# Kernel tuning notes

Measured on AMD Instinct MI355X. Metric: run time of the kernel, lower is better.

The kernel has to match this reference:

```python
import jax, jax.numpy as jnp
import numpy as np

B, T, C, D = 8, 4096, 1024, 128  # batch, seq_len, n_embd, attn_dim


def setup_inputs() -> dict:
    key = jax.random.key(0)
    kx, kq, kk, kv = jax.random.split(key, 4)
    scale = 0.02
    return {
        "x": jax.random.normal(kx, (B, T, C), dtype=jnp.float32),
        "Wq": jax.random.normal(kq, (C, D), dtype=jnp.float32) * scale,
        "Wk": jax.random.normal(kk, (C, D), dtype=jnp.float32) * scale,
        "Wv": jax.random.normal(kv, (C, D), dtype=jnp.float32) * scale,
    }


def reference(x, Wq, Wk, Wv):
    # single-head causal self-attention (dropout in eval mode -> identity)
    q = jnp.einsum("btc,cd->btd", x, Wq)
    k = jnp.einsum("btc,cd->btd", x, Wk)
    v = jnp.einsum("btc,cd->btd", x, Wv)
    dk = q.shape[-1]
    scores = jnp.einsum("btd,bsd->bts", q, k) / jnp.sqrt(jnp.float32(dk))  # [B,T,T]
    tq = q.shape[1]
    causal = jnp.tril(jnp.ones((tq, tq), dtype=bool))
    scores = jnp.where(causal[None, :, :], scores, jnp.float32(-jnp.inf))
    weights = jax.nn.softmax(scores, axis=-1)
    return jnp.einsum("bts,bsd->btd", weights, v)
```

## Files before the change

### kernel.cpp

```cpp
#include <hip/hip_runtime.h>
#include <hip/hip_bf16.h>
#include <stdint.h>


typedef __attribute__((ext_vector_type(8))) short short8;
typedef __attribute__((ext_vector_type(4))) float f32x4;
typedef __attribute__((ext_vector_type(4))) unsigned short u16x4;

#define NB 8
#define NT 4096
#define NC 1024
#define ND 128

__device__ __forceinline__ unsigned short f2bf(float f) {
    union { float f; uint32_t u; } v; v.f = f;
    uint32_t u = v.u;
    return (unsigned short)((u + 0x7FFFu + ((u >> 16) & 1u)) >> 16);
}

__global__ void prep_w(const float* __restrict__ Wq, const float* __restrict__ Wk,
                       const float* __restrict__ Wv, unsigned short* __restrict__ Wbt) {
    int idx = blockIdx.x * 256 + threadIdx.x;
    int w = idx >> 17;
    int rem = idx & 131071;
    int n = rem >> 10;
    int k = rem & 1023;
    const float* W = (w == 0) ? Wq : (w == 1) ? Wk : Wv;
    Wbt[idx] = f2bf(W[k * ND + n]);
}

__global__ __launch_bounds__(256, 3)
void qkv_gemm(const float* __restrict__ x, const unsigned short* __restrict__ Wbt,
              unsigned short* __restrict__ Qo, unsigned short* __restrict__ Ko,
              unsigned short* __restrict__ Vto) {
    __shared__ __align__(16) float Al[128 * 64];
    __shared__ __align__(16) unsigned short Bl[128 * 64];
    const int mt = blockIdx.x, nt = blockIdx.y;
    const int tid = threadIdx.x;
    const int lane = tid & 63;
    const int w = tid >> 6;
    const int wr = w >> 1, wc = w & 1;
    const int l15 = lane & 15, lg = lane >> 4;
    const int m0 = mt * 128;
    const unsigned short* Wn = Wbt + (size_t)nt * (ND * NC);

    f32x4 acc[4][4];
#pragma unroll
    for (int i = 0; i < 4; ++i)
#pragma unroll
        for (int j = 0; j < 4; ++j) acc[i][j] = (f32x4)0.0f;

    for (int ks = 0; ks < 16; ++ks) {
        const int k0 = ks * 64;
#pragma unroll
        for (int r = 0; r < 8; ++r) {
            int o = r * 4096 + tid * 16;
            int row = o >> 8;
            int colb = (o & 255) ^ ((row & 7) << 4);
            const float* src = x + (size_t)(m0 + row) * NC + k0 + (colb >> 2);
            __builtin_amdgcn_global_load_lds(
                (const __attribute__((address_space(1))) void*)src,
                (__attribute__((address_space(3))) void*)((char*)Al + o), 16, 0, 0);
        }
#pragma unroll
        for (int r = 0; r < 4; ++r) {
            int o = r * 4096 + tid * 16;
            int row = o >> 7;
            int colb = (o & 127) ^ ((row & 7) << 4);
            const unsigned short* src = Wn + (size_t)row * NC + k0 + (colb >> 1);
            __builtin_amdgcn_global_load_lds(
                (const __attribute__((address_space(1))) void*)src,
                (__attribute__((address_space(3))) void*)((char*)Bl + o), 16, 0, 0);
        }
        __syncthreads();

#pragma unroll
        for (int kc = 0; kc < 2; ++kc) {
            short8 a[4], b[4];
#pragma unroll
            for (int mi = 0; mi < 4; ++mi) {
                const int row = wr * 64 + mi * 16 + l15;
                const int cb = (row & 7) << 4;
                const int base = row * 256;
                f32x4 lo = *reinterpret_cast<const f32x4*>(
                    (const char*)Al + base + ((kc * 128 + lg * 32) ^ cb));
                f32x4 hi = *reinterpret_cast<const f32x4*>(
                    (const char*)Al + base + ((kc * 128 + lg * 32 + 16) ^ cb));
                short8 av;
#pragma unroll
                for (int e = 0; e < 4; ++e) {
                    av[e] = (short)f2bf(lo[e]);
                    av[4 + e] = (short)f2bf(hi[e]);
                }
                a[mi] = av;
            }
#pragma unroll
            for (int ni = 0; ni < 4; ++ni) {
                const int row = wc * 64 + ni * 16 + l15;
                const int cb = (row & 7) << 4;
                b[ni] = *reinterpret_cast<const short8*>(
                    (const char*)Bl + row * 128 + ((kc * 64 + lg * 16) ^ cb));
            }
#pragma unroll
            for (int mi = 0; mi < 4; ++mi)
#pragma unroll
                for (int ni = 0; ni < 4; ++ni)
                    acc[mi][ni] = __builtin_amdgcn_mfma_f32_16x16x32_bf16(
                        a[mi], b[ni], acc[mi][ni], 0, 0, 0);
        }
        __syncthreads();
    }
#pragma unroll
    for (int mi = 0; mi < 4; ++mi)
#pragma unroll
        for (int ni = 0; ni < 4; ++ni)
#pragma unroll
            for (int r = 0; r < 4; ++r) {
                int row = m0 + wr * 64 + mi * 16 + lg * 4 + r;
                int col = wc * 64 + ni * 16 + l15;
                float v = acc[mi][ni][r];
                if (nt == 0) v *= 0.08838834764831845f;
                unsigned short bv = f2bf(v);
                if (nt == 0) Qo[(size_t)row * ND + col] = bv;
                else if (nt == 1) Ko[(size_t)row * ND + col] = bv;
                else {
                    int bb2 = row >> 12, t = row & 4095;
                    Vto[((size_t)(bb2 * ND + col)) * NT + t] = bv;
                }
            }
}

__global__ __launch_bounds__(512, 2)
void attn_fwd(const unsigned short* __restrict__ Q, const unsigned short* __restrict__ K,
              const unsigned short* __restrict__ Vt, float* __restrict__ out) {
    __shared__ __align__(16) char smem[149504];

    const int bid = blockIdx.x;
    const int p = bid >> 3, b = bid & 7;
    const int tid = threadIdx.x;
    const int w = tid >> 6, lane = tid & 63;
    const int l15 = lane & 15, lg = lane >> 4;
    const int g = w >> 2, wq = w & 3;

    const float L2E = 1.4426950408889634f;

    unsigned short* Kg = (unsigned short*)(smem + g * 32768);
    unsigned short* Vg = (unsigned short*)(smem + 65536 + g * 32768);
    unsigned short* pw = (unsigned short*)(smem + 131072 + w * 2304);
    float* mOp = (float*)(smem) + wq * 2048;
    float* mml = (float*)(smem + 32768) + wq * 32;

    const unsigned short* Kbase = &K[(size_t)b * NT * ND];
    const unsigned short* Vbase = &Vt[(size_t)b * ND * NT];

    auto stage = [&](int buf, int s0) {
#pragma unroll
        for (int r = 0; r < 4; ++r) {
            int off = r * 4096 + wq * 1024 + lane * 16;
            int row = off >> 8;
            int gcol = (off & 255) ^ ((row & 7) << 4);
            const unsigned short* src = Kbase + (size_t)(s0 + row) * ND + (gcol >> 1);
            __builtin_amdgcn_global_load_lds(
                (const __attribute__((address_space(1))) void*)src,
                (__attribute__((address_space(3))) void*)(Kg + ((buf * 16384 + r * 4096 + wq * 1024) >> 1)),
                16, 0, 0);
        }
#pragma unroll
        for (int r = 0; r < 4; ++r) {
            int off = r * 4096 + wq * 1024 + lane * 16;
            int row = off >> 7;
            int gcol = (off & 127) ^ ((row & 7) << 4);
            const unsigned short* src = Vbase + (size_t)row * NT + s0 + (gcol >> 1);
            __builtin_amdgcn_global_load_lds(
                (const __attribute__((address_space(1))) void*)src,
                (__attribute__((address_space(3))) void*)(Vg + ((buf * 16384 + r * 4096 + wq * 1024) >> 1)),
                16, 0, 0);
        }
    };

    for (int half = 0; half < 2; ++half) {
        const int qt = half ? (63 - p) : p;
        const int qb0 = qt * 64;
        const int qw0 = qb0 + wq * 16;
        const int niter = (qt + 2) >> 1;

        short8 qf[4];
        const size_t qbase = ((size_t)b * NT + qw0 + l15) * ND;
#pragma unroll
        for (int c = 0; c < 4; ++c)
            qf[c] = *reinterpret_cast<const short8*>(&Q[qbase + c * 32 + lg * 8]);

        f32x4 o[8];
#pragma unroll
        for (int jn = 0; jn < 8; ++jn) o[jn] = (f32x4)0.0f;
        float mrow = -1e30f, lsum = 0.0f;

        if (g <= qt) stage(0, g * 64);
        __syncthreads();
        int cur = 0;

        for (int i = 0; i < niter; ++i) {
            const int t = 2 * i + g;
            const int s0 = t * 64;
            if (t + 2 <= qt) stage(cur ^ 1, (t + 2) * 64);

            if (t <= qt) {
                const unsigned short* KlC = Kg + cur * 8192;
                f32x4 s[4];
#pragma unroll
                for (int j = 0; j < 4; ++j) s[j] = (f32x4)0.0f;
                __builtin_amdgcn_s_setprio(1);
#pragma unroll
                for (int j = 0; j < 4; ++j) {
                    const int row = j * 16 + l15;
                    const int cb = (row & 7) << 4;
#pragma unroll
                    for (int c = 0; c < 4; ++c) {
                        short8 kf = *reinterpret_cast<const short8*>(
                            &KlC[row * 128 + (((c * 64 + lg * 16) ^ cb) >> 1)]);
                        s[j] = __builtin_amdgcn_mfma_f32_16x16x32_bf16(kf, qf[c], s[j], 0, 0, 0);
                    }
                }
                __builtin_amdgcn_s_setprio(0);

                const unsigned short* VlC = Vg + cur * 8192;
                short8 vf0[8];
#pragma unroll
                for (int jn = 0; jn < 4; ++jn) {
                    const int row = jn * 16 + l15;
                    const int cb = (row & 7) << 4;
#pragma unroll
                    for (int kc = 0; kc < 2; ++kc)
                        vf0[jn * 2 + kc] = *reinterpret_cast<const short8*>(
                            &VlC[row * 64 + (((kc * 64 + lg * 16) ^ cb) >> 1)]);
                }

                const bool diag = (s0 + 64 > qw0);
                float pmax = -1e30f;
                if (diag) {
#pragma unroll
                    for (int j = 0; j < 4; ++j)
#pragma unroll
                        for (int r = 0; r < 4; ++r) {
                            float sv = s[j][r];
                            if (s0 + j * 16 + lg * 4 + r > qw0 + l15) sv = -1e30f;
                            s[j][r] = sv;
                            pmax = fmaxf(pmax, sv);
                        }
                } else {
#pragma unroll
                    for (int j = 0; j < 4; ++j)
#pragma unroll
                        for (int r = 0; r < 4; ++r)
                            pmax = fmaxf(pmax, s[j][r]);
                }
                pmax = fmaxf(pmax, __shfl_xor(pmax, 16, 64));
                pmax = fmaxf(pmax, __shfl_xor(pmax, 32, 64));
                const bool need = (pmax > mrow + 8.0f);
                float mn = need ? pmax : mrow;
                float alpha = need ? exp2f((mrow - mn) * L2E) : 1.0f;
                mrow = mn;
                float psum = 0.0f;
#pragma unroll
                for (int j = 0; j < 4; ++j)
#pragma unroll
                    for (int r = 0; r < 4; ++r) {
                        float pv = exp2f((s[j][r] - mn) * L2E);
                        s[j][r] = pv;
                        psum += pv;
                    }
                psum += __shfl_xor(psum, 16, 64);
                psum += __shfl_xor(psum, 32, 64);
                lsum = lsum * alpha + psum;

#pragma unroll
                for (int j = 0; j < 4; ++j) {
                    uint2 val;
                    asm("v_cvt_pk_bf16_f32 %0, %1, %2"
                        : "=v"(val.x) : "v"(s[j][0]), "v"(s[j][1]));
                    asm("v_cvt_pk_bf16_f32 %0, %1, %2"
                        : "=v"(val.y) : "v"(s[j][2]), "v"(s[j][3]));
                    *reinterpret_cast<uint2*>(&pw[l15 * 72 + j * 16 + lg * 4]) = val;
                }
                asm volatile("s_waitcnt lgkmcnt(0)" ::: "memory");
                short8 pa[2];
#pragma unroll
                for (int kc = 0; kc < 2; ++kc)
                    pa[kc] = *reinterpret_cast<const short8*>(&pw[l15 * 72 + kc * 32 + lg * 8]);
                asm volatile("s_waitcnt lgkmcnt(0)" ::: "memory");

                if (__any((int)need)) {
                    float aT[4];
#pragma unroll
                    for (int r = 0; r < 4; ++r) aT[r] = __shfl(alpha, lg * 4 + r, 64);
#pragma unroll
                    for (int jn = 0; jn < 8; ++jn)
#pragma unroll
                        for (int r = 0; r < 4; ++r) o[jn][r] *= aT[r];
                }

                __builtin_amdgcn_s_setprio(1);
#pragma unroll
                for (int jn = 0; jn < 4; ++jn)
#pragma unroll
                    for (int kc = 0; kc < 2; ++kc)
                        o[jn] = __builtin_amdgcn_mfma_f32_16x16x32_bf16(
                            pa[kc], vf0[jn * 2 + kc], o[jn], 0, 0, 0);
#pragma unroll
                for (int jn = 4; jn < 8; ++jn) {
                    const int row = jn * 16 + l15;
                    const int cb = (row & 7) << 4;
#pragma unroll
                    for (int kc = 0; kc < 2; ++kc) {
                        short8 vf = *reinterpret_cast<const short8*>(
                            &VlC[row * 64 + (((kc * 64 + lg * 16) ^ cb) >> 1)]);
                        o[jn] = __builtin_amdgcn_mfma_f32_16x16x32_bf16(pa[kc], vf, o[jn], 0, 0, 0);
                    }
                }
                __builtin_amdgcn_s_setprio(0);
            }

            __syncthreads();
            cur ^= 1;
        }

        if (g == 1) {
#pragma unroll
            for (int jn = 0; jn < 8; ++jn)
#pragma unroll
                for (int r = 0; r < 4; ++r)
                    mOp[(lg * 4 + r) * 128 + jn * 16 + l15] = o[jn][r];
            if (lg == 0) {
                mml[l15] = mrow;
                mml[16 + l15] = lsum;
            }
        }
        __syncthreads();
        if (g == 0) {
            float e0[4], e1[4], rL[4];
#pragma unroll
            for (int r = 0; r < 4; ++r) {
                int rr = lg * 4 + r;
                float m0T = __shfl(mrow, rr, 64);
                float l0T = __shfl(lsum, rr, 64);
                float m1 = mml[rr], l1 = mml[16 + rr];
                float M = fmaxf(m0T, m1);
                e0[r] = exp2f((m0T - M) * L2E);
                e1[r] = exp2f((m1 - M) * L2E);
                rL[r] = 1.0f / (l0T * e0[r] + l1 * e1[r]);
            }
#pragma unroll
            for (int jn = 0; jn < 8; ++jn)
#pragma unroll
                for (int r = 0; r < 4; ++r) {
                    int rr = lg * 4 + r, cc = jn * 16 + l15;
                    float v = o[jn][r] * e0[r] + mOp[rr * 128 + cc] * e1[r];
                    out[((size_t)b * NT + qw0 + rr) * ND + cc] = v * rL[r];
                }
        }
        __syncthreads();
    }
}

extern "C" void kernel_launch(void* const* d_in, const int* in_sizes, int n_in,
                              void* d_out, int out_size, void* d_ws, size_t ws_size,
                              hipStream_t stream) {
    const float* x  = (const float*)d_in[0];
    const float* Wq = (const float*)d_in[1];
    const float* Wk = (const float*)d_in[2];
    const float* Wv = (const float*)d_in[3];
    float* out = (float*)d_out;

    unsigned short* ws  = (unsigned short*)d_ws;
    unsigned short* Wbt = ws;
    unsigned short* Qb  = Wbt + 3 * ND * NC;
    unsigned short* Kb  = Qb + (size_t)NB * NT * ND;
    unsigned short* Vtb = Kb + (size_t)NB * NT * ND;

    prep_w<<<1536, 256, 0, stream>>>(Wq, Wk, Wv, Wbt);
    qkv_gemm<<<dim3(256, 3), 256, 0, stream>>>(x, Wbt, Qb, Kb, Vtb);
    attn_fwd<<<256, 512, 0, stream>>>(Qb, Kb, Vtb, out);
}
```

Measured before the change: 130.3 us.

## Software-pipeline softmax/PV of previous tile behind QK^T of current tile

Restructures the attention inner loop so each iteration first runs softmax and the PV MFMAs for the previously computed score tile, then computes QK^T for the current tile and preloads all V fragments into registers. The aim is to overlap the MFMA score computation with the exp/reduction work, hiding latency within each wave. It raises register pressure (16 V fragments plus carried scores), which risks lower occupancy or spills.

```diff
diff --git a/kernel.cpp b/kernel.cpp
--- a/kernel.cpp
+++ b/kernel.cpp
@@ -195,6 +195,114 @@
         for (int jn = 0; jn < 8; ++jn) o[jn] = (f32x4)0.0f;
         float mrow = -1e30f, lsum = 0.0f;
 
+        f32x4 sp[4];
+        short8 vfp[16];
+        int s0p = -1;
+
+        auto QKT = [&](const unsigned short* KlC) {
+#pragma unroll
+            for (int j = 0; j < 4; ++j) sp[j] = (f32x4)0.0f;
+            __builtin_amdgcn_s_setprio(1);
+#pragma unroll
+            for (int j = 0; j < 4; ++j) {
+                const int row = j * 16 + l15;
+                const int cb = (row & 7) << 4;
+#pragma unroll
+                for (int c = 0; c < 4; ++c) {
+                    short8 kf = *reinterpret_cast<const short8*>(
+                        &KlC[row * 128 + (((c * 64 + lg * 16) ^ cb) >> 1)]);
+                    sp[j] = __builtin_amdgcn_mfma_f32_16x16x32_bf16(kf, qf[c], sp[j], 0, 0, 0);
+                }
+            }
+            __builtin_amdgcn_s_setprio(0);
+        };
+        auto readVF = [&](const unsigned short* VlC) {
+#pragma unroll
+            for (int jn = 0; jn < 8; ++jn) {
+                const int row = jn * 16 + l15;
+                const int cb = (row & 7) << 4;
+#pragma unroll
+                for (int kc = 0; kc < 2; ++kc)
+                    vfp[jn * 2 + kc] = *reinterpret_cast<const short8*>(
+                        &VlC[row * 64 + (((kc * 64 + lg * 16) ^ cb) >> 1)]);
+            }
+        };
+        auto SMPV = [&]() {
+            const int s0c = s0p;
+            const bool diag = (s0c + 64 > qw0);
+            float pmax = -1e30f;
+            if (diag) {
+#pragma unroll
+                for (int j = 0; j < 4; ++j)
+#pragma unroll
+                    for (int r = 0; r < 4; ++r) {
+                        float sv = sp[j][r];
+                        if (s0c + j * 16 + lg * 4 + r > qw0 + l15) sv = -1e30f;
+                        sp[j][r] = sv;
+                        pmax = fmaxf(pmax, sv);
+                    }
+            } else {
+#pragma unroll
+                for (int j = 0; j < 4; ++j)
+#pragma unroll
+                    for (int r = 0; r < 4; ++r)
+                        pmax = fmaxf(pmax, sp[j][r]);
+            }
+            pmax = fmaxf(pmax, __shfl_xor(pmax, 16, 64));
+            pmax = fmaxf(pmax, __shfl_xor(pmax, 32, 64));
+            const bool need = (pmax > mrow + 8.0f);
+            float mn = need ? pmax : mrow;
+            float alpha = need ? exp2f((mrow - mn) * L2E) : 1.0f;
+            mrow = mn;
+            float psum = 0.0f;
+#pragma unroll
+            for (int j = 0; j < 4; ++j)
+#pragma unroll
+                for (int r = 0; r < 4; ++r) {
+                    float pv = exp2f((sp[j][r] - mn) * L2E);
+                    sp[j][r] = pv;
+                    psum += pv;
+                }
+            psum += __shfl_xor(psum, 16, 64);
+            psum += __shfl_xor(psum, 32, 64);
+            lsum = lsum * alpha + psum;
+
+#pragma unroll
+            for (int j = 0; j < 4; ++j) {
+                uint2 val;
+                asm("v_cvt_pk_bf16_f32 %0, %1, %2"
+                    : "=v"(val.x) : "v"(sp[j][0]), "v"(sp[j][1]));
+                asm("v_cvt_pk_bf16_f32 %0, %1, %2"
+                    : "=v"(val.y) : "v"(sp[j][2]), "v"(sp[j][3]));
+                *reinterpret_cast<uint2*>(&pw[l15 * 72 + j * 16 + lg * 4]) = val;
+            }
+            asm volatile("s_waitcnt lgkmcnt(0)" ::: "memory");
+            short8 pa[2];
+#pragma unroll
+            for (int kc = 0; kc < 2; ++kc)
+                pa[kc] = *reinterpret_cast<const short8*>(&pw[l15 * 72 + kc * 32 + lg * 8]);
+            asm volatile("s_waitcnt lgkmcnt(0)" ::: "memory");
+
+            if (__any((int)need)) {
+                float aT[4];
+#pragma unroll
+                for (int r = 0; r < 4; ++r) aT[r] = __shfl(alpha, lg * 4 + r, 64);
+#pragma unroll
+                for (int jn = 0; jn < 8; ++jn)
+#pragma unroll
+                    for (int r = 0; r < 4; ++r) o[jn][r] *= aT[r];
+            }
+
+            __builtin_amdgcn_s_setprio(1);
+#pragma unroll
+            for (int jn = 0; jn < 8; ++jn)
+#pragma unroll
+                for (int kc = 0; kc < 2; ++kc)
+                    o[jn] = __builtin_amdgcn_mfma_f32_16x16x32_bf16(
+                        pa[kc], vfp[jn * 2 + kc], o[jn], 0, 0, 0);
+            __builtin_amdgcn_s_setprio(0);
+        };
+
         if (g <= qt) stage(0, g * 64);
         __syncthreads();
         int cur = 0;
@@ -204,125 +312,20 @@
             const int s0 = t * 64;
             if (t + 2 <= qt) stage(cur ^ 1, (t + 2) * 64);
 
+            if (s0p >= 0) SMPV();
+
             if (t <= qt) {
-                const unsigned short* KlC = Kg + cur * 8192;
-                f32x4 s[4];
-#pragma unroll
-                for (int j = 0; j < 4; ++j) s[j] = (f32x4)0.0f;
-                __builtin_amdgcn_s_setprio(1);
-#pragma unroll
-                for (int j = 0; j < 4; ++j) {
-                    const int row = j * 16 + l15;
-                    const int cb = (row & 7) << 4;
-#pragma unroll
-                    for (int c = 0; c < 4; ++c) {
-                        short8 kf = *reinterpret_cast<const short8*>(
-                            &KlC[row * 128 + (((c * 64 + lg * 16) ^ cb) >> 1)]);
-                        s[j] = __builtin_amdgcn_mfma_f32_16x16x32_bf16(kf, qf[c], s[j], 0, 0, 0);
-                    }
-                }
-                __builtin_amdgcn_s_setprio(0);
-
-                const unsigned short* VlC = Vg + cur * 8192;
-                short8 vf0[8];
-#pragma unroll
-                for (int jn = 0; jn < 4; ++jn) {
-                    const int row = jn * 16 + l15;
-                    const int cb = (row & 7) << 4;
-#pragma unroll
-                    for (int kc = 0; kc < 2; ++kc)
-                        vf0[jn * 2 + kc] = *reinterpret_cast<const short8*>(
-                            &VlC[row * 64 + (((kc * 64 + lg * 16) ^ cb) >> 1)]);
-                }
-
-                const bool diag = (s0 + 64 > qw0);
-                float pmax = -1e30f;
-                if (diag) {
-#pragma unroll
-                    for (int j = 0; j < 4; ++j)
-#pragma unroll
-                        for (int r = 0; r < 4; ++r) {
-                            float sv = s[j][r];
-                            if (s0 + j * 16 + lg * 4 + r > qw0 + l15) sv = -1e30f;
-                            s[j][r] = sv;
-                            pmax = fmaxf(pmax, sv);
-                        }
-                } else {
-#pragma unroll
-                    for (int j = 0; j < 4; ++j)
-#pragma unroll
-                        for (int r = 0; r < 4; ++r)
-                            pmax = fmaxf(pmax, s[j][r]);
-                }
-                pmax = fmaxf(pmax, __shfl_xor(pmax, 16, 64));
-                pmax = fmaxf(pmax, __shfl_xor(pmax, 32, 64));
-                const bool need = (pmax > mrow + 8.0f);
-                float mn = need ? pmax : mrow;
-                float alpha = need ? exp2f((mrow - mn) * L2E) : 1.0f;
-                mrow = mn;
-                float psum = 0.0f;
-#pragma unroll
-                for (int j = 0; j < 4; ++j)
-#pragma unroll
-                    for (int r = 0; r < 4; ++r) {
-                        float pv = exp2f((s[j][r] - mn) * L2E);
-                        s[j][r] = pv;
-                        psum += pv;
-                    }
-                psum += __shfl_xor(psum, 16, 64);
-                psum += __shfl_xor(psum, 32, 64);
-                lsum = lsum * alpha + psum;
-
-#pragma unroll
-                for (int j = 0; j < 4; ++j) {
-                    uint2 val;
-                    asm("v_cvt_pk_bf16_f32 %0, %1, %2"
-                        : "=v"(val.x) : "v"(s[j][0]), "v"(s[j][1]));
-                    asm("v_cvt_pk_bf16_f32 %0, %1, %2"
-                        : "=v"(val.y) : "v"(s[j][2]), "v"(s[j][3]));
-                    *reinterpret_cast<uint2*>(&pw[l15 * 72 + j * 16 + lg * 4]) = val;
-                }
-                asm volatile("s_waitcnt lgkmcnt(0)" ::: "memory");
-                short8 pa[2];
-#pragma unroll
-                for (int kc = 0; kc < 2; ++kc)
-                    pa[kc] = *reinterpret_cast<const short8*>(&pw[l15 * 72 + kc * 32 + lg * 8]);
-                asm volatile("s_waitcnt lgkmcnt(0)" ::: "memory");
-
-                if (__any((int)need)) {
-                    float aT[4];
-#pragma unroll
-                    for (int r = 0; r < 4; ++r) aT[r] = __shfl(alpha, lg * 4 + r, 64);
-#pragma unroll
-                    for (int jn = 0; jn < 8; ++jn)
-#pragma unroll
-                        for (int r = 0; r < 4; ++r) o[jn][r] *= aT[r];
-                }
-
-                __builtin_amdgcn_s_setprio(1);
-#pragma unroll
-                for (int jn = 0; jn < 4; ++jn)
-#pragma unroll
-                    for (int kc = 0; kc < 2; ++kc)
-                        o[jn] = __builtin_amdgcn_mfma_f32_16x16x32_bf16(
-                            pa[kc], vf0[jn * 2 + kc], o[jn], 0, 0, 0);
-#pragma unroll
-                for (int jn = 4; jn < 8; ++jn) {
-                    const int row = jn * 16 + l15;
-                    const int cb = (row & 7) << 4;
-#pragma unroll
-                    for (int kc = 0; kc < 2; ++kc) {
-                        short8 vf = *reinterpret_cast<const short8*>(
-                            &VlC[row * 64 + (((kc * 64 + lg * 16) ^ cb) >> 1)]);
-                        o[jn] = __builtin_amdgcn_mfma_f32_16x16x32_bf16(pa[kc], vf, o[jn], 0, 0, 0);
-                    }
-                }
-                __builtin_amdgcn_s_setprio(0);
+                QKT(Kg + cur * 8192);
+                readVF(Vg + cur * 8192);
+                s0p = s0;
+            } else {
+                s0p = -1;
             }
 
             __syncthreads();
             cur ^= 1;
         }
+        if (s0p >= 0) SMPV();
 
         if (g == 1) {
 #pragma unroll
```

Result: slower. 136.8 us (+5.0%).

## Fuse Q/K/V projections per block so each x tile is loaded once

Applied to the files above, without the earlier changes.

The QKV GEMM now computes all three projections in one block with a 64-row M tile and a 384-wide N tile, instead of launching a separate grid slice per projection. The goal is to read the fp32 x activations (the dominant traffic) and convert them to bf16 only once instead of three times. The cost is more weight traffic per block, a larger LDS footprint (48KB of weights plus 16KB of x), more accumulator registers, and lower occupancy (launch bounds drop from 3 to 2).

```diff
diff --git a/kernel.cpp b/kernel.cpp
--- a/kernel.cpp
+++ b/kernel.cpp
@@ -29,31 +29,32 @@
     Wbt[idx] = f2bf(W[k * ND + n]);
 }
 
-__global__ __launch_bounds__(256, 3)
+__global__ __launch_bounds__(256, 2)
 void qkv_gemm(const float* __restrict__ x, const unsigned short* __restrict__ Wbt,
               unsigned short* __restrict__ Qo, unsigned short* __restrict__ Ko,
               unsigned short* __restrict__ Vto) {
-    __shared__ __align__(16) float Al[128 * 64];
-    __shared__ __align__(16) unsigned short Bl[128 * 64];
-    const int mt = blockIdx.x, nt = blockIdx.y;
+    __shared__ __align__(16) float Al[64 * 64];
+    __shared__ __align__(16) unsigned short Bl[3 * 128 * 64];
+    const int mt = blockIdx.x;
     const int tid = threadIdx.x;
     const int lane = tid & 63;
     const int w = tid >> 6;
     const int wr = w >> 1, wc = w & 1;
     const int l15 = lane & 15, lg = lane >> 4;
-    const int m0 = mt * 128;
-    const unsigned short* Wn = Wbt + (size_t)nt * (ND * NC);
-
-    f32x4 acc[4][4];
-#pragma unroll
-    for (int i = 0; i < 4; ++i)
-#pragma unroll
-        for (int j = 0; j < 4; ++j) acc[i][j] = (f32x4)0.0f;
+    const int m0 = mt * 64;
+
+    f32x4 acc[3][2][4];
+#pragma unroll
+    for (int nt = 0; nt < 3; ++nt)
+#pragma unroll
+        for (int mi = 0; mi < 2; ++mi)
+#pragma unroll
+            for (int ni = 0; ni < 4; ++ni) acc[nt][mi][ni] = (f32x4)0.0f;
 
     for (int ks = 0; ks < 16; ++ks) {
         const int k0 = ks * 64;
 #pragma unroll
-        for (int r = 0; r < 8; ++r) {
+        for (int r = 0; r < 4; ++r) {
             int o = r * 4096 + tid * 16;
             int row = o >> 8;
             int colb = (o & 255) ^ ((row & 7) << 4);
@@ -63,11 +64,14 @@
                 (__attribute__((address_space(3))) void*)((char*)Al + o), 16, 0, 0);
         }
 #pragma unroll
-        for (int r = 0; r < 4; ++r) {
+        for (int r = 0; r < 12; ++r) {
             int o = r * 4096 + tid * 16;
-            int row = o >> 7;
-            int colb = (o & 127) ^ ((row & 7) << 4);
-            const unsigned short* src = Wn + (size_t)row * NC + k0 + (colb >> 1);
+            int nt = o >> 14;
+            int within = o & 16383;
+            int row = within >> 7;
+            int colb = (within & 127) ^ ((row & 7) << 4);
+            const unsigned short* src = Wbt + (size_t)nt * (ND * NC)
+                                      + (size_t)row * NC + k0 + (colb >> 1);
             __builtin_amdgcn_global_load_lds(
                 (const __attribute__((address_space(1))) void*)src,
                 (__attribute__((address_space(3))) void*)((char*)Bl + o), 16, 0, 0);
@@ -76,10 +80,10 @@
 
 #pragma unroll
         for (int kc = 0; kc < 2; ++kc) {
-            short8 a[4], b[4];
-#pragma unroll
-            for (int mi = 0; mi < 4; ++mi) {
-                const int row = wr * 64 + mi * 16 + l15;
+            short8 a[2];
+#pragma unroll
+            for (int mi = 0; mi < 2; ++mi) {
+                const int row = wr * 32 + mi * 16 + l15;
                 const int cb = (row & 7) << 4;
                 const int base = row * 256;
                 f32x4 lo = *reinterpret_cast<const f32x4*>(
@@ -95,39 +99,42 @@
                 a[mi] = av;
             }
 #pragma unroll
-            for (int ni = 0; ni < 4; ++ni) {
-                const int row = wc * 64 + ni * 16 + l15;
-                const int cb = (row & 7) << 4;
-                b[ni] = *reinterpret_cast<const short8*>(
-                    (const char*)Bl + row * 128 + ((kc * 64 + lg * 16) ^ cb));
-            }
-#pragma unroll
-            for (int mi = 0; mi < 4; ++mi)
-#pragma unroll
-                for (int ni = 0; ni < 4; ++ni)
-                    acc[mi][ni] = __builtin_amdgcn_mfma_f32_16x16x32_bf16(
-                        a[mi], b[ni], acc[mi][ni], 0, 0, 0);
+            for (int nt = 0; nt < 3; ++nt)
+#pragma unroll
+                for (int ni = 0; ni < 4; ++ni) {
+                    const int row = wc * 64 + ni * 16 + l15;
+                    const int cb = (row & 7) << 4;
+                    short8 bb = *reinterpret_cast<const short8*>(
+                        (const char*)Bl + nt * 16384 + row * 128
+                        + ((kc * 64 + lg * 16) ^ cb));
+                    acc[nt][0][ni] = __builtin_amdgcn_mfma_f32_16x16x32_bf16(
+                        a[0], bb, acc[nt][0][ni], 0, 0, 0);
+                    acc[nt][1][ni] = __builtin_amdgcn_mfma_f32_16x16x32_bf16(
+                        a[1], bb, acc[nt][1][ni], 0, 0, 0);
+                }
         }
         __syncthreads();
     }
 #pragma unroll
-    for (int mi = 0; mi < 4; ++mi)
-#pragma unroll
-        for (int ni = 0; ni < 4; ++ni)
-#pragma unroll
-            for (int r = 0; r < 4; ++r) {
-                int row = m0 + wr * 64 + mi * 16 + lg * 4 + r;
-                int col = wc * 64 + ni * 16 + l15;
-                float v = acc[mi][ni][r];
-                if (nt == 0) v *= 0.08838834764831845f;
-                unsigned short bv = f2bf(v);
-                if (nt == 0) Qo[(size_t)row * ND + col] = bv;
-                else if (nt == 1) Ko[(size_t)row * ND + col] = bv;
-                else {
-                    int bb2 = row >> 12, t = row & 4095;
-                    Vto[((size_t)(bb2 * ND + col)) * NT + t] = bv;
-                }
-            }
+    for (int nt = 0; nt < 3; ++nt)
+#pragma unroll
+        for (int mi = 0; mi < 2; ++mi)
+#pragma unroll
+            for (int ni = 0; ni < 4; ++ni)
+#pragma unroll
+                for (int r = 0; r < 4; ++r) {
+                    int row = m0 + wr * 32 + mi * 16 + lg * 4 + r;
+                    int col = wc * 64 + ni * 16 + l15;
+                    float v = acc[nt][mi][ni][r];
+                    if (nt == 0) v *= 0.08838834764831845f;
+                    unsigned short bv = f2bf(v);
+                    if (nt == 0) Qo[(size_t)row * ND + col] = bv;
+                    else if (nt == 1) Ko[(size_t)row * ND + col] = bv;
+                    else {
+                        int bb2 = row >> 12, t = row & 4095;
+                        Vto[((size_t)(bb2 * ND + col)) * NT + t] = bv;
+                    }
+                }
 }
 
 __global__ __launch_bounds__(512, 2)
@@ -378,6 +385,6 @@
     unsigned short* Vtb = Kb + (size_t)NB * NT * ND;
 
     prep_w<<<1536, 256, 0, stream>>>(Wq, Wk, Wv, Wbt);
-    qkv_gemm<<<dim3(256, 3), 256, 0, stream>>>(x, Wbt, Qb, Kb, Vtb);
+    qkv_gemm<<<512, 256, 0, stream>>>(x, Wbt, Qb, Kb, Vtb);
     attn_fwd<<<256, 512, 0, stream>>>(Qb, Kb, Vtb, out);
 }
```

Measured after the change: 123.1 us. 1.06x faster.
